# Kernel tuning notes

Hardware: AMD Instinct MI355X
Metric: run time of the kernel (lower is better)

## Reference

```python
import jax, jax.numpy as jnp
import numpy as np

N, E, G = 2048, 4096, 16
IN_DIM, HID, E_DIM, EDGE_H = 11, 128, 6, 64
EPS = 1e-5


def setup_inputs() -> dict:
    key = jax.random.key(0)
    ks = jax.random.split(key, 32)
    s = 0.1  # keep activations tame
    inp = {
        "h": jax.random.normal(ks[0], (N, IN_DIM), jnp.float32),
        "e": jax.random.normal(ks[1], (E, E_DIM), jnp.float32),
        "src": jax.random.randint(ks[2], (E,), 0, N, jnp.int32),
        "dst": jax.random.randint(ks[3], (E,), 0, N, jnp.int32),
        "node_graph": (jnp.arange(N, dtype=jnp.int32) // (N // G)),
        # layer 0 (in_dim=11 -> hid=128)
        "eW1_0": jax.random.normal(ks[4], (E_DIM, EDGE_H), jnp.float32) * s,
        "eb1_0": jax.random.normal(ks[5], (EDGE_H,), jnp.float32) * s,
        "eW2_0": jax.random.normal(ks[6], (EDGE_H, IN_DIM * HID), jnp.float32) * s,
        "eb2_0": jax.random.normal(ks[7], (IN_DIM * HID,), jnp.float32) * s,
        "bias_0": jax.random.normal(ks[8], (HID,), jnp.float32) * s,
        "gamma_0": jax.random.uniform(ks[9], (HID,), jnp.float32, 0.5, 1.5),
        "beta_0": jax.random.normal(ks[10], (HID,), jnp.float32) * s,
        "mean_0": jax.random.normal(ks[11], (HID,), jnp.float32) * s,
        "var_0": jax.random.uniform(ks[12], (HID,), jnp.float32, 0.5, 1.5),
        # layers 1..3 stacked (hid -> hid)
        "eW1": jax.random.normal(ks[13], (3, E_DIM, EDGE_H), jnp.float32) * s,
        "eb1": jax.random.normal(ks[14], (3, EDGE_H), jnp.float32) * s,
        "eW2": jax.random.normal(ks[15], (3, EDGE_H, HID * HID), jnp.float32) * s,
        "eb2": jax.random.normal(ks[16], (3, HID * HID), jnp.float32) * s,
        "bias": jax.random.normal(ks[17], (3, HID), jnp.float32) * s,
        "gamma": jax.random.uniform(ks[18], (3, HID), jnp.float32, 0.5, 1.5),
        "beta": jax.random.normal(ks[19], (3, HID), jnp.float32) * s,
        "mean": jax.random.normal(ks[20], (3, HID), jnp.float32) * s,
        "var": jax.random.uniform(ks[21], (3, HID), jnp.float32, 0.5, 1.5),
        # output BN (on mean readout)
        "g_out": jax.random.uniform(ks[22], (HID,), jnp.float32, 0.5, 1.5),
        "b_out": jax.random.normal(ks[23], (HID,), jnp.float32) * s,
        "m_out": jax.random.normal(ks[24], (HID,), jnp.float32) * s,
        "v_out": jax.random.uniform(ks[25], (HID,), jnp.float32, 0.5, 1.5),
    }
    return inp


def _bn(x, ga, be, mu, vv):
    return (x - mu) * jax.lax.rsqrt(vv + EPS) * ga + be


def _nn_layer(x, e, src, dst, W1, b1, W2, b2, bb, ga, be, mu, vv, din):
    # edge MLP -> per-edge weight matrix [E, din, HID]
    w = (jax.nn.relu(e @ W1 + b1) @ W2 + b2).reshape(E, din, HID)
    msg = jnp.einsum('ei,eio->eo', x[src], w)          # per-edge message [E, HID]
    agg = jax.ops.segment_sum(msg, dst, num_segments=N)
    deg = jax.ops.segment_sum(jnp.ones((E,), x.dtype), dst, num_segments=N)
    agg = agg / jnp.maximum(deg, 1.0)[:, None] + bb    # mean aggregation + NNConv bias
    return _bn(jax.nn.relu(agg), ga, be, mu, vv)       # relu -> BatchNorm (eval)


def reference(h, e, src, dst, node_graph, eW1_0, eb1_0, eW2_0, eb2_0, bias_0,
              gamma_0, beta_0, mean_0, var_0, eW1, eb1, eW2, eb2, bias,
              gamma, beta, mean, var, g_out, b_out, m_out, v_out):
    x = _nn_layer(h, e, src, dst, eW1_0, eb1_0, eW2_0, eb2_0, bias_0,
                  gamma_0, beta_0, mean_0, var_0, IN_DIM)
    for i in range(3):
        x = _nn_layer(x, e, src, dst, eW1[i], eb1[i], eW2[i], eb2[i], bias[i],
                      gamma[i], beta[i], mean[i], var[i], HID)
    # dropout is identity in eval mode
    cnt = jax.ops.segment_sum(jnp.ones((N,), x.dtype), node_graph, num_segments=G)
    hn = jax.ops.segment_sum(x, node_graph, num_segments=G) / cnt[:, None]
    hx = jax.ops.segment_max(x, node_graph, num_segments=G)
    hn = _bn(hn, g_out, b_out, m_out, v_out)
    return jnp.concatenate([hn, hx], axis=1)  # [G, 2*HID]
```

## Files before the change

kernel.cpp:

```cpp
#include <hip/hip_runtime.h>
#include <stdint.h>

#define N_NODES 2048
#define N_EDGES 4096
#define N_GRAPH 16
#define IN_DIM  11
#define HID     128
#define E_DIMF  6
#define EDGE_H  64
#define NSLICE  65
#define ZCOLS   (NSLICE*HID)
#define BN_EPS  1e-5f

typedef __attribute__((ext_vector_type(8))) short short8;
typedef __attribute__((ext_vector_type(4))) float f32x4;

static __device__ __forceinline__ float bf2f(unsigned short u) {
  union { float f; uint32_t i; } x; x.i = ((uint32_t)u) << 16; return x.f;
}
static __device__ __forceinline__ unsigned short f2bf(float f) {
  union { float f; uint32_t i; } x; x.f = f;
  uint32_t i = x.i;
  return (unsigned short)((i + 0x7FFFu + ((i >> 16) & 1u)) >> 16);
}

struct PrepP {
  const float *eW2_0, *eb2_0, *eW2, *eb2, *h_in;
  const int *dst;
  unsigned short *WbT0, *WbTL, *xb0;
  int *roff, *elist;
  float *gsum;
  unsigned int *gmax;
  float *gcnt;
};

#define PREP_BLOCKS 270
__global__ __launch_bounds__(256) void prep_all(PrepP p) {
  const int bid = blockIdx.x, t = threadIdx.x;
  __shared__ union {
    struct { int hist[N_NODES]; int part[256]; } csr;
    unsigned short tile[128 * 130];
  } sm;

  if (bid == 0) {
    for (int i = t; i < N_NODES; i += 256) sm.csr.hist[i] = 0;
    __syncthreads();
    for (int e = t; e < N_EDGES; e += 256) atomicAdd(&sm.csr.hist[p.dst[e]], 1);
    __syncthreads();
    const int base = t * 8;
    int loc[8];
    int s = 0;
#pragma unroll
    for (int j = 0; j < 8; ++j) { loc[j] = s; s += sm.csr.hist[base + j]; }
    sm.csr.part[t] = s;
    __syncthreads();
    for (int d = 1; d < 256; d <<= 1) {
      int v = sm.csr.part[t];
      if (t >= d) v += sm.csr.part[t - d];
      __syncthreads();
      sm.csr.part[t] = v;
      __syncthreads();
    }
    const int pre = (t == 0) ? 0 : sm.csr.part[t - 1];
#pragma unroll
    for (int j = 0; j < 8; ++j) p.roff[base + j] = pre + loc[j];
    if (t == 255) p.roff[N_NODES] = pre + s;
    __syncthreads();
#pragma unroll
    for (int j = 0; j < 8; ++j) sm.csr.hist[base + j] = pre + loc[j];
    __syncthreads();
    for (int e = t; e < N_EDGES; e += 256) {
      int pos = atomicAdd(&sm.csr.hist[p.dst[e]], 1);
      p.elist[pos] = e;
    }
  } else if (bid <= 260) {
    const int s = bid - 1;
    if (s < 65) {
      const int k = s;
      const float* srcp = (k < 64) ? (p.eW2_0 + (size_t)k * IN_DIM * HID) : p.eb2_0;
      for (int j = t; j < IN_DIM * HID; j += 256) {
        int i = j >> 7, o = j & 127;
        sm.tile[i * 130 + o] = f2bf(srcp[j]);
      }
      __syncthreads();
      for (int j = t; j < HID * 32; j += 256) {
        int o = j >> 5, i = j & 31;
        p.WbT0[((size_t)k * HID + o) * 32 + i] =
            (i < IN_DIM) ? sm.tile[i * 130 + o] : (unsigned short)0;
      }
    } else {
      const int sl = s - 65, l = sl / 65, k = sl % 65;
      const float* srcp = (k < 64) ? (p.eW2 + ((size_t)l * 64 + k) * (HID * HID))
                                   : (p.eb2 + (size_t)l * (HID * HID));
      unsigned short* dstp = p.WbTL + (size_t)l * ZCOLS * HID;
      for (int j = t; j < HID * HID; j += 256) {
        int i = j >> 7, o = j & 127;
        sm.tile[i * 130 + o] = f2bf(srcp[j]);
      }
      __syncthreads();
      for (int j = t; j < HID * HID; j += 256) {
        int o = j >> 7, i = j & 127;
        dstp[((size_t)k * HID + o) * HID + i] = sm.tile[i * 130 + o];
      }
    }
  } else if (bid <= 268) {
    for (int idx = (bid - 261) * 256 + t; idx < N_NODES * 32; idx += 8 * 256) {
      int n = idx >> 5, i = idx & 31;
      p.xb0[idx] = f2bf(i < IN_DIM ? p.h_in[n * IN_DIM + i] : 0.f);
    }
  } else {
    for (int i = t; i < N_GRAPH * HID; i += 256) {
      p.gsum[i] = 0.f;
      p.gmax[i] = 0u;
    }
    if (t < N_GRAPH) p.gcnt[t] = 0.f;
  }
}

template <int KP, int SWZ>
__global__ __launch_bounds__(256) void gemm_z(const unsigned short* __restrict__ Xb,
                                              const unsigned short* __restrict__ WbT,
                                              unsigned short* __restrict__ Z) {
  extern __shared__ unsigned short lds[];
  unsigned short* Al = lds;
  unsigned short* Bl = lds + 128 * KP;
  const int nb = blockIdx.x;
  const int mb = blockIdx.y;
  const int t = threadIdx.x;
  const int ROWB = KP * 2;
  const int NCH = 128 * ROWB / 16;
  const unsigned short* Asrc = Xb + (size_t)mb * 128 * KP;
  const unsigned short* Bsrc = WbT + (size_t)nb * 128 * KP;
  for (int c = t; c < NCH; c += 256) {
    int off = c * 16;
    int row = off / ROWB;
    int kb = off % ROWB;
    int dsto = row * ROWB + (kb ^ ((row & SWZ) << 4));
    *(uint4*)((char*)Al + dsto) = *(const uint4*)((const char*)Asrc + off);
    *(uint4*)((char*)Bl + dsto) = *(const uint4*)((const char*)Bsrc + off);
  }
  __syncthreads();
  const int w = t >> 6, l = t & 63;
  const int wm = (w >> 1) * 64, wn = (w & 1) * 64;
  const int lr = l & 15, lh = l >> 4;
  f32x4 acc[4][4] = {};
#pragma unroll
  for (int kk = 0; kk < KP; kk += 32) {
    short8 a[4], b[4];
    const int kb = (kk + lh * 8) * 2;
#pragma unroll
    for (int mi = 0; mi < 4; ++mi) {
      int row = wm + mi * 16 + lr;
      int addr = row * ROWB + (kb ^ ((row & SWZ) << 4));
      a[mi] = *(const short8*)((const char*)Al + addr);
    }
#pragma unroll
    for (int ni = 0; ni < 4; ++ni) {
      int col = wn + ni * 16 + lr;
      int addr = col * ROWB + (kb ^ ((col & SWZ) << 4));
      b[ni] = *(const short8*)((const char*)Bl + addr);
    }
#pragma unroll
    for (int mi = 0; mi < 4; ++mi)
#pragma unroll
      for (int ni = 0; ni < 4; ++ni)
        acc[mi][ni] = __builtin_amdgcn_mfma_f32_16x16x32_bf16(b[ni], a[mi], acc[mi][ni], 0, 0, 0);
  }
#pragma unroll
  for (int mi = 0; mi < 4; ++mi) {
    const int node = mb * 128 + wm + mi * 16 + lr;
    unsigned short* zp = Z + (size_t)node * ZCOLS + nb * 128 + wn + lh * 4;
#pragma unroll
    for (int ni = 0; ni < 4; ++ni) {
      ushort4 pk;
      pk.x = f2bf(acc[mi][ni][0]);
      pk.y = f2bf(acc[mi][ni][1]);
      pk.z = f2bf(acc[mi][ni][2]);
      pk.w = f2bf(acc[mi][ni][3]);
      *(ushort4*)(zp + ni * 16) = pk;
    }
  }
}

template <int LAST>
__global__ __launch_bounds__(128) void node_gather(
    const float* __restrict__ efeat, const float* __restrict__ W1,
    const float* __restrict__ b1, const unsigned short* __restrict__ Z,
    const int* __restrict__ elist, const int* __restrict__ roff,
    const int* __restrict__ src,
    const float* __restrict__ bias, const float* __restrict__ gamma,
    const float* __restrict__ beta, const float* __restrict__ mean,
    const float* __restrict__ var,
    unsigned short* __restrict__ xbout,
    const int* __restrict__ ng, float* __restrict__ gsum,
    unsigned int* __restrict__ gmax, float* __restrict__ gcnt) {
  const int n = blockIdx.x, t = threadIdx.x;
  const int cg2 = t & 15, kg = t >> 4;
  const int start = roff[n], end = roff[n + 1];
  __shared__ float red[128][9];
  float acc8[8] = {};
  for (int idx = start; idx < end; ++idx) {
    const int e = elist[idx];
    const int se = src[e];
    float ef[E_DIMF];
#pragma unroll
    for (int j = 0; j < E_DIMF; ++j) ef[j] = efeat[e * E_DIMF + j];
    float hk[8];
#pragma unroll
    for (int kk = 0; kk < 8; ++kk) {
      const int k = kg * 8 + kk;
      float a = b1[k];
#pragma unroll
      for (int j = 0; j < E_DIMF; ++j) a += ef[j] * W1[j * EDGE_H + k];
      hk[kk] = fmaxf(a, 0.f);
    }
    const unsigned short* zr = Z + (size_t)se * ZCOLS + cg2 * 8;
#pragma unroll
    for (int kk = 0; kk < 8; ++kk) {
      short8 v = *(const short8*)(zr + (kg * 8 + kk) * HID);
      const float hv = hk[kk];
#pragma unroll
      for (int j = 0; j < 8; ++j) acc8[j] += hv * bf2f((unsigned short)v[j]);
    }
    if (kg == 0) {
      short8 v = *(const short8*)(zr + 64 * HID);
#pragma unroll
      for (int j = 0; j < 8; ++j) acc8[j] += bf2f((unsigned short)v[j]);
    }
  }
#pragma unroll
  for (int j = 0; j < 8; ++j) red[t][j] = acc8[j];
  __syncthreads();
  const int o = t;
  float s = 0.f;
#pragma unroll
  for (int k2 = 0; k2 < 8; ++k2) s += red[k2 * 16 + (o >> 3)][o & 7];
  const int dg = end - start;
  float v = s / (float)(dg > 0 ? dg : 1) + bias[o];
  v = fmaxf(v, 0.f);
  v = (v - mean[o]) * rsqrtf(var[o] + BN_EPS) * gamma[o] + beta[o];
  if (!LAST) {
    xbout[n * HID + o] = f2bf(v);
  } else {
    const int g = ng[n];
    atomicAdd(&gsum[g * HID + o], v);
    unsigned int u = __float_as_uint(v);
    unsigned int key = (u & 0x80000000u) ? ~u : (u | 0x80000000u);
    atomicMax(&gmax[g * HID + o], key);
    if (o == 0) atomicAdd(&gcnt[g], 1.f);
  }
}

__global__ void out_final(const float* __restrict__ gsum, const unsigned int* __restrict__ gmax,
                          const float* __restrict__ gcnt,
                          const float* __restrict__ g_out, const float* __restrict__ b_out,
                          const float* __restrict__ m_out, const float* __restrict__ v_out,
                          float* __restrict__ out) {
  int g = blockIdx.x, t = threadIdx.x;
  float hn = gsum[g * HID + t] / fmaxf(gcnt[g], 1.0f);
  hn = (hn - m_out[t]) * rsqrtf(v_out[t] + BN_EPS) * g_out[t] + b_out[t];
  unsigned int key = gmax[g * HID + t];
  unsigned int u = (key & 0x80000000u) ? (key ^ 0x80000000u) : ~key;
  out[g * 2 * HID + t] = hn;
  out[g * 2 * HID + HID + t] = __uint_as_float(u);
}


extern "C" void kernel_launch(void* const* d_in, const int* in_sizes, int n_in,
                              void* d_out, int out_size, void* d_ws, size_t ws_size,
                              hipStream_t stream) {
  const float* h_in   = (const float*)d_in[0];
  const float* e_in   = (const float*)d_in[1];
  const int*   src    = (const int*)d_in[2];
  const int*   dst    = (const int*)d_in[3];
  const int*   ng     = (const int*)d_in[4];
  const float* eW1_0  = (const float*)d_in[5];
  const float* eb1_0  = (const float*)d_in[6];
  const float* eW2_0  = (const float*)d_in[7];
  const float* eb2_0  = (const float*)d_in[8];
  const float* bias_0 = (const float*)d_in[9];
  const float* gamma_0= (const float*)d_in[10];
  const float* beta_0 = (const float*)d_in[11];
  const float* mean_0 = (const float*)d_in[12];
  const float* var_0  = (const float*)d_in[13];
  const float* eW1    = (const float*)d_in[14];
  const float* eb1    = (const float*)d_in[15];
  const float* eW2    = (const float*)d_in[16];
  const float* eb2    = (const float*)d_in[17];
  const float* biasL  = (const float*)d_in[18];
  const float* gammaL = (const float*)d_in[19];
  const float* betaL  = (const float*)d_in[20];
  const float* meanL  = (const float*)d_in[21];
  const float* varL   = (const float*)d_in[22];
  const float* g_out  = (const float*)d_in[23];
  const float* b_out  = (const float*)d_in[24];
  const float* m_out  = (const float*)d_in[25];
  const float* v_out  = (const float*)d_in[26];
  float* out = (float*)d_out;

  char* ws = (char*)d_ws;
  size_t off = 0;
  auto alloc = [&](size_t bytes) {
    void* pp = ws + off;
    off = (off + bytes + 255) & ~(size_t)255;
    return pp;
  };
  unsigned short* Z    = (unsigned short*)alloc((size_t)N_NODES * ZCOLS * 2);
  unsigned short* WbT0 = (unsigned short*)alloc((size_t)ZCOLS * 32 * 2);
  unsigned short* WbTL = (unsigned short*)alloc((size_t)3 * ZCOLS * HID * 2);
  unsigned short* xb0  = (unsigned short*)alloc((size_t)N_NODES * 32 * 2);
  unsigned short* xb   = (unsigned short*)alloc((size_t)N_NODES * HID * 2);
  float* gsum          = (float*)alloc((size_t)N_GRAPH * HID * 4);
  unsigned int* gmax   = (unsigned int*)alloc((size_t)N_GRAPH * HID * 4);
  float* gcnt          = (float*)alloc((size_t)N_GRAPH * 4);
  int* roff            = (int*)alloc((size_t)(N_NODES + 1) * 4);
  int* elist           = (int*)alloc((size_t)N_EDGES * 4);

  PrepP P;
  P.eW2_0 = eW2_0; P.eb2_0 = eb2_0; P.eW2 = eW2; P.eb2 = eb2; P.h_in = h_in;
  P.dst = dst;
  P.WbT0 = WbT0; P.WbTL = WbTL; P.xb0 = xb0;
  P.roff = roff; P.elist = elist;
  P.gsum = gsum; P.gmax = gmax; P.gcnt = gcnt;

  prep_all<<<PREP_BLOCKS, 256, 0, stream>>>(P);

  gemm_z<32, 3><<<dim3(65, 16), 256, 2 * 128 * 32 * 2, stream>>>(xb0, WbT0, Z);
  node_gather<0><<<N_NODES, 128, 0, stream>>>(e_in, eW1_0, eb1_0, Z, elist, roff, src,
                                              bias_0, gamma_0, beta_0, mean_0, var_0,
                                              xb, ng, gsum, gmax, gcnt);

  for (int l = 0; l < 3; ++l) {
    gemm_z<128, 7><<<dim3(65, 16), 256, 2 * 128 * 128 * 2, stream>>>(
        xb, WbTL + (size_t)l * ZCOLS * HID, Z);
    if (l < 2)
      node_gather<0><<<N_NODES, 128, 0, stream>>>(
          e_in, eW1 + l * E_DIMF * EDGE_H, eb1 + l * EDGE_H, Z, elist, roff, src,
          biasL + l * HID, gammaL + l * HID, betaL + l * HID, meanL + l * HID,
          varL + l * HID, xb, ng, gsum, gmax, gcnt);
    else
      node_gather<1><<<N_NODES, 128, 0, stream>>>(
          e_in, eW1 + l * E_DIMF * EDGE_H, eb1 + l * EDGE_H, Z, elist, roff, src,
          biasL + l * HID, gammaL + l * HID, betaL + l * HID, meanL + l * HID,
          varL + l * HID, xb, ng, gsum, gmax, gcnt);
  }

  out_final<<<N_GRAPH, HID, 0, stream>>>(gsum, gmax, gcnt, g_out, b_out, m_out,
                                         v_out, out);
}
```

Measured before the change: 182.9 us.

## Use direct global-to-LDS loads in GEMM and pre-permute edge data for gather

```diff
diff --git a/kernel.cpp b/kernel.cpp
--- a/kernel.cpp
+++ b/kernel.cpp
@@ -24,11 +24,18 @@
   return (unsigned short)((i + 0x7FFFu + ((i >> 16) & 1u)) >> 16);
 }
 
+static __device__ __forceinline__ void gload_lds16(const void* g, void* l) {
+  __builtin_amdgcn_global_load_lds(
+      (const __attribute__((address_space(1))) uint32_t*)g,
+      (__attribute__((address_space(3))) uint32_t*)l, 16, 0, 0);
+}
+
 struct PrepP {
-  const float *eW2_0, *eb2_0, *eW2, *eb2, *h_in;
-  const int *dst;
+  const float *eW2_0, *eb2_0, *eW2, *eb2, *h_in, *efeat;
+  const int *dst, *srcv;
   unsigned short *WbT0, *WbTL, *xb0;
-  int *roff, *elist;
+  int *roff, *elist, *esrc;
+  float *ef6;
   float *gsum;
   unsigned int *gmax;
   float *gcnt;
@@ -72,6 +79,13 @@
     for (int e = t; e < N_EDGES; e += 256) {
       int pos = atomicAdd(&sm.csr.hist[p.dst[e]], 1);
       p.elist[pos] = e;
+    }
+    __syncthreads();
+    for (int i = t; i < N_EDGES; i += 256) {
+      const int e = p.elist[i];
+      p.esrc[i] = p.srcv[e];
+#pragma unroll
+      for (int j = 0; j < E_DIMF; ++j) p.ef6[i * E_DIMF + j] = p.efeat[e * E_DIMF + j];
     }
   } else if (bid <= 260) {
     const int s = bid - 1;
@@ -132,12 +146,11 @@
   const unsigned short* Asrc = Xb + (size_t)mb * 128 * KP;
   const unsigned short* Bsrc = WbT + (size_t)nb * 128 * KP;
   for (int c = t; c < NCH; c += 256) {
-    int off = c * 16;
-    int row = off / ROWB;
-    int kb = off % ROWB;
-    int dsto = row * ROWB + (kb ^ ((row & SWZ) << 4));
-    *(uint4*)((char*)Al + dsto) = *(const uint4*)((const char*)Asrc + off);
-    *(uint4*)((char*)Bl + dsto) = *(const uint4*)((const char*)Bsrc + off);
+    const int d = c * 16;
+    const int row = d / ROWB;
+    const int s = d ^ ((row & SWZ) << 4);
+    gload_lds16((const char*)Asrc + s, (char*)Al + d);
+    gload_lds16((const char*)Bsrc + s, (char*)Bl + d);
   }
   __syncthreads();
   const int w = t >> 6, l = t & 63;
@@ -183,28 +196,28 @@
 }
 
 template <int LAST>
-__global__ __launch_bounds__(128) void node_gather(
-    const float* __restrict__ efeat, const float* __restrict__ W1,
+__global__ __launch_bounds__(256) void node_gather(
+    const float* __restrict__ ef6, const float* __restrict__ W1,
     const float* __restrict__ b1, const unsigned short* __restrict__ Z,
-    const int* __restrict__ elist, const int* __restrict__ roff,
-    const int* __restrict__ src,
+    const int* __restrict__ esrc, const int* __restrict__ roff,
     const float* __restrict__ bias, const float* __restrict__ gamma,
     const float* __restrict__ beta, const float* __restrict__ mean,
     const float* __restrict__ var,
     unsigned short* __restrict__ xbout,
     const int* __restrict__ ng, float* __restrict__ gsum,
     unsigned int* __restrict__ gmax, float* __restrict__ gcnt) {
-  const int n = blockIdx.x, t = threadIdx.x;
-  const int cg2 = t & 15, kg = t >> 4;
+  const int t = threadIdx.x;
+  const int hh = t >> 7, tt = t & 127;
+  const int n = blockIdx.x * 2 + hh;
+  const int cg2 = tt & 15, kg = tt >> 4;
   const int start = roff[n], end = roff[n + 1];
-  __shared__ float red[128][9];
+  __shared__ float red[2][128][9];
   float acc8[8] = {};
   for (int idx = start; idx < end; ++idx) {
-    const int e = elist[idx];
-    const int se = src[e];
+    const int se = esrc[idx];
     float ef[E_DIMF];
 #pragma unroll
-    for (int j = 0; j < E_DIMF; ++j) ef[j] = efeat[e * E_DIMF + j];
+    for (int j = 0; j < E_DIMF; ++j) ef[j] = ef6[idx * E_DIMF + j];
     float hk[8];
 #pragma unroll
     for (int kk = 0; kk < 8; ++kk) {
@@ -229,12 +242,12 @@
     }
   }
 #pragma unroll
-  for (int j = 0; j < 8; ++j) red[t][j] = acc8[j];
+  for (int j = 0; j < 8; ++j) red[hh][tt][j] = acc8[j];
   __syncthreads();
-  const int o = t;
+  const int o = tt;
   float s = 0.f;
 #pragma unroll
-  for (int k2 = 0; k2 < 8; ++k2) s += red[k2 * 16 + (o >> 3)][o & 7];
+  for (int k2 = 0; k2 < 8; ++k2) s += red[hh][k2 * 16 + (o >> 3)][o & 7];
   const int dg = end - start;
   float v = s / (float)(dg > 0 ? dg : 1) + bias[o];
   v = fmaxf(v, 0.f);
@@ -315,32 +328,35 @@
   float* gcnt          = (float*)alloc((size_t)N_GRAPH * 4);
   int* roff            = (int*)alloc((size_t)(N_NODES + 1) * 4);
   int* elist           = (int*)alloc((size_t)N_EDGES * 4);
+  int* esrc            = (int*)alloc((size_t)N_EDGES * 4);
+  float* ef6           = (float*)alloc((size_t)N_EDGES * E_DIMF * 4);
 
   PrepP P;
   P.eW2_0 = eW2_0; P.eb2_0 = eb2_0; P.eW2 = eW2; P.eb2 = eb2; P.h_in = h_in;
-  P.dst = dst;
+  P.efeat = e_in;
+  P.dst = dst; P.srcv = src;
   P.WbT0 = WbT0; P.WbTL = WbTL; P.xb0 = xb0;
-  P.roff = roff; P.elist = elist;
+  P.roff = roff; P.elist = elist; P.esrc = esrc; P.ef6 = ef6;
   P.gsum = gsum; P.gmax = gmax; P.gcnt = gcnt;
 
   prep_all<<<PREP_BLOCKS, 256, 0, stream>>>(P);
 
   gemm_z<32, 3><<<dim3(65, 16), 256, 2 * 128 * 32 * 2, stream>>>(xb0, WbT0, Z);
-  node_gather<0><<<N_NODES, 128, 0, stream>>>(e_in, eW1_0, eb1_0, Z, elist, roff, src,
-                                              bias_0, gamma_0, beta_0, mean_0, var_0,
-                                              xb, ng, gsum, gmax, gcnt);
+  node_gather<0><<<N_NODES / 2, 256, 0, stream>>>(ef6, eW1_0, eb1_0, Z, esrc, roff,
+                                                  bias_0, gamma_0, beta_0, mean_0,
+                                                  var_0, xb, ng, gsum, gmax, gcnt);
 
   for (int l = 0; l < 3; ++l) {
     gemm_z<128, 7><<<dim3(65, 16), 256, 2 * 128 * 128 * 2, stream>>>(
         xb, WbTL + (size_t)l * ZCOLS * HID, Z);
     if (l < 2)
-      node_gather<0><<<N_NODES, 128, 0, stream>>>(
-          e_in, eW1 + l * E_DIMF * EDGE_H, eb1 + l * EDGE_H, Z, elist, roff, src,
+      node_gather<0><<<N_NODES / 2, 256, 0, stream>>>(
+          ef6, eW1 + l * E_DIMF * EDGE_H, eb1 + l * EDGE_H, Z, esrc, roff,
           biasL + l * HID, gammaL + l * HID, betaL + l * HID, meanL + l * HID,
           varL + l * HID, xb, ng, gsum, gmax, gcnt);
     else
-      node_gather<1><<<N_NODES, 128, 0, stream>>>(
-          e_in, eW1 + l * E_DIMF * EDGE_H, eb1 + l * EDGE_H, Z, elist, roff, src,
+      node_gather<1><<<N_NODES / 2, 256, 0, stream>>>(
+          ef6, eW1 + l * E_DIMF * EDGE_H, eb1 + l * EDGE_H, Z, esrc, roff,
           biasL + l * HID, gammaL + l * HID, betaL + l * HID, meanL + l * HID,
           varL + l * HID, xb, ng, gsum, gmax, gcnt);
   }
```

Result: slower. 205.7 us (+12.4%).
